# Optimization experiments

Hardware: AMD Instinct MI355X
Metric: run time of the kernel (lower is better)

Reference implementation:

```python
import jax, jax.numpy as jnp
import numpy as np

N_INT4, N_INT8, K, GROUP = 6144, 2048, 8192, 128
N_TOTAL = N_INT4 + N_INT8
M = 16


def setup_inputs() -> dict:
    key = jax.random.key(0)
    ks = jax.random.split(key, 8)
    x = jax.random.normal(ks[0], (M, K), jnp.float32)
    # uint4 weights: values 0..15 (stored int32)
    w_int4 = jax.random.randint(ks[1], (N_INT4, K), 0, 16, jnp.int32)
    # group-wise scales [N_int4, K//group_size]
    s_int4 = jax.random.uniform(ks[2], (N_INT4, K // GROUP), jnp.float32, minval=0.005, maxval=0.02)
    # int8 weights stored in offset-128 form (w_int8 + 128 -> 0..255), as pack_for_marlin builds
    w_uint8 = jax.random.randint(ks[3], (N_INT8, K), 0, 256, jnp.int32)
    # per-channel int8 scales
    s_int8 = jax.random.uniform(ks[4], (N_INT8,), jnp.float32, minval=0.005, maxval=0.02)
    awq_scales = jax.random.uniform(ks[5], (K,), jnp.float32, minval=0.5, maxval=2.0)
    bias = jax.random.normal(ks[6], (N_TOTAL,), jnp.float32) * 0.01
    inv_perm = jax.random.permutation(ks[7], N_TOTAL).astype(jnp.int32)
    return dict(x=x, w_int4=w_int4, s_int4=s_int4, w_uint8=w_uint8, s_int8=s_int8,
                awq_scales=awq_scales, bias=bias, inv_perm=inv_perm, group_size=GROUP)


def reference(x, w_int4, s_int4, w_uint8, s_int8, awq_scales, bias, inv_perm, group_size):
    dt = x.dtype
    k = x.shape[-1]
    # AWQ input scaling (unfused path: x / awq_scales)
    x2 = x.reshape(-1, k) / awq_scales[None, :]
    sum_x = jnp.sum(x2, axis=1, keepdims=True)  # [M, 1]

    # Marlin uint4b8 dequant: (q - 8) * scale, group-wise scales for int4 rows
    s4_k = jnp.repeat(s_int4, group_size, axis=1)            # [N4, K]
    W4 = (w_int4.astype(dt) - 8.0) * s4_k                    # [N4, K]

    # int8 rows split into high/low nibbles with scales 16*s and s
    high = (w_uint8 >> 4) & 15
    low = w_uint8 & 15
    Wh = (high.astype(dt) - 8.0) * (16.0 * s_int8)[:, None]  # [N8, K]
    Wl = (low.astype(dt) - 8.0) * s_int8[:, None]            # [N8, K]

    Wc = jnp.concatenate([W4, Wh, Wl], axis=0)               # [N4+2*N8, K]
    y = x2 @ Wc.T                                            # marlin_gemm equivalent

    n4 = W4.shape[0]
    n8 = s_int8.shape[0]
    y4 = y[:, :n4]
    # int8 reconstruction: y_high + y_low + 8*s_int8*sum_x  == s_int8 * (x @ w_int8^T)
    y8 = y[:, n4:n4 + n8] + y[:, n4 + n8:] + (8.0 * s_int8)[None, :] * sum_x
    y_out = jnp.concatenate([y4, y8], axis=-1)[:, inv_perm] + bias[None, :]
    return y_out.reshape(*x.shape[:-1], n4 + n8)
```

## Files before the change

### kernel.cpp

```cpp
#include <hip/hip_runtime.h>
#include <hip/hip_bf16.h>

constexpr int K    = 8192;
constexpr int N4   = 6144;
constexpr int N8   = 2048;
constexpr int NT   = N4 + N8;
constexpr int NG   = K / 128;
constexpr int SPLITS = 16;
constexpr int CPS    = 16;

typedef short  short8  __attribute__((ext_vector_type(8)));
typedef float  floatx4 __attribute__((ext_vector_type(4)));

__device__ inline short f2bf(float f) {
    __hip_bfloat16 h = __float2bfloat16(f);
    return __builtin_bit_cast(short, h);
}

__global__ void prep_kernel(const float* __restrict__ x,
                            const float* __restrict__ awq,
                            const int*   __restrict__ inv_perm,
                            const float* __restrict__ bias,
                            short* __restrict__ x2bf,
                            int*   __restrict__ fwd,
                            float* __restrict__ out) {
    const int tid  = blockIdx.x * blockDim.x + threadIdx.x;
    const int c    = tid >> 9;
    const int rem  = tid & 511;
    const int lane = rem >> 3;
    const int j    = rem & 7;
    const int m    = lane & 15;
    const int k    = c * 32 + (lane >> 4) * 8 + j;
    x2bf[tid] = f2bf(x[m * K + k] / awq[k]);
    out[tid]  = bias[tid & (NT - 1)];
    if (tid < NT) fwd[inv_perm[tid]] = tid;
}

__global__ __launch_bounds__(256)
void qgemv_kernel(const short* __restrict__ xf,
                  const int*   __restrict__ w4,
                  const float* __restrict__ s4,
                  const int*   __restrict__ w8,
                  const float* __restrict__ s8,
                  const int*   __restrict__ fwd,
                  float* __restrict__ out) {
    const int t    = threadIdx.x;
    const int lane = t & 63;
    const int wid  = blockIdx.x * 4 + (t >> 6);
    const int tile = wid >> 4;
    const int spl  = wid & (SPLITS - 1);
    const int nb   = tile * 16;
    const int i    = lane & 15;
    const int q    = lane >> 4;
    const int row  = nb + i;

    const bool is4 = (nb < N4);
    const int* wr  = is4 ? (w4 + (size_t)row * K + q * 8)
                         : (w8 + (size_t)(row - N4) * K + q * 8);
    const int c0   = spl * CPS;

    floatx4 acc = {0.f, 0.f, 0.f, 0.f};

    #pragma unroll 1
    for (int gi = 0; gi < 4; ++gi) {
        const int g   = (c0 >> 2) + gi;
        const float s  = is4 ? s4[row * NG + g] : 1.f;
        const float sb = is4 ? -8.f * s : -128.f;

        #pragma unroll
        for (int ci = 0; ci < 4; ++ci) {
            const int c = c0 + gi * 4 + ci;
            const int4 wa = *(const int4*)(wr + (size_t)c * 32);
            const int4 wb = *(const int4*)(wr + (size_t)c * 32 + 4);

            short8 bfrag;
            bfrag[0] = f2bf((float)wa.x * s + sb);
            bfrag[1] = f2bf((float)wa.y * s + sb);
            bfrag[2] = f2bf((float)wa.z * s + sb);
            bfrag[3] = f2bf((float)wa.w * s + sb);
            bfrag[4] = f2bf((float)wb.x * s + sb);
            bfrag[5] = f2bf((float)wb.y * s + sb);
            bfrag[6] = f2bf((float)wb.z * s + sb);
            bfrag[7] = f2bf((float)wb.w * s + sb);

            const short8 afrag = *(const short8*)(xf + (size_t)c * 512 + lane * 8);

            acc = __builtin_amdgcn_mfma_f32_16x16x32_bf16(afrag, bfrag, acc, 0, 0, 0);
        }
    }

    const float sc = is4 ? 1.f : s8[row - N4];
    const int   d  = fwd[row];
    #pragma unroll
    for (int r = 0; r < 4; ++r) {
        const int m = q * 4 + r;
        unsafeAtomicAdd(&out[(size_t)m * NT + d], acc[r] * sc);
    }
}

extern "C" void kernel_launch(void* const* d_in, const int* in_sizes, int n_in,
                              void* d_out, int out_size, void* d_ws, size_t ws_size,
                              hipStream_t stream) {
    const float* x        = (const float*)d_in[0];
    const int*   w_int4   = (const int*)  d_in[1];
    const float* s_int4   = (const float*)d_in[2];
    const int*   w_uint8  = (const int*)  d_in[3];
    const float* s_int8   = (const float*)d_in[4];
    const float* awq      = (const float*)d_in[5];
    const float* bias     = (const float*)d_in[6];
    const int*   inv_perm = (const int*)  d_in[7];

    short* x2bf = (short*)d_ws;
    int*   fwd  = (int*)((char*)d_ws + (size_t)16 * K * sizeof(short));

    prep_kernel<<<(16 * K) / 256, 256, 0, stream>>>(x, awq, inv_perm, bias,
                                                    x2bf, fwd, (float*)d_out);
    qgemv_kernel<<<2048, 256, 0, stream>>>(x2bf, w_int4, s_int4,
                                           w_uint8, s_int8, fwd,
                                           (float*)d_out);
}
```

Measured before the change: 370.5 us.

## Reduce split-K within a block via LDS and double-buffer loads

Each block now owns one 16-row tile and splits K across its four waves. Partial sums are reduced through shared memory instead of global atomics, and the bias add moves from the prep kernel into the final store. The main loop double-buffers weight and activation loads per scale group to overlap memory with dequant and MFMA work. The grid shrinks from 2048 to 512 blocks, so each wave streams a longer K range. That cuts parallelism and may leave fewer loads in flight for this bandwidth-bound read of int32 weights.

```diff
diff --git a/kernel.cpp b/kernel.cpp
--- a/kernel.cpp
+++ b/kernel.cpp
@@ -6,8 +6,6 @@
 constexpr int N8   = 2048;
 constexpr int NT   = N4 + N8;
 constexpr int NG   = K / 128;
-constexpr int SPLITS = 16;
-constexpr int CPS    = 16;
 
 typedef short  short8  __attribute__((ext_vector_type(8)));
 typedef float  floatx4 __attribute__((ext_vector_type(4)));
@@ -20,10 +18,8 @@
 __global__ void prep_kernel(const float* __restrict__ x,
                             const float* __restrict__ awq,
                             const int*   __restrict__ inv_perm,
-                            const float* __restrict__ bias,
                             short* __restrict__ x2bf,
-                            int*   __restrict__ fwd,
-                            float* __restrict__ out) {
+                            int*   __restrict__ fwd) {
     const int tid  = blockIdx.x * blockDim.x + threadIdx.x;
     const int c    = tid >> 9;
     const int rem  = tid & 511;
@@ -32,7 +28,6 @@
     const int m    = lane & 15;
     const int k    = c * 32 + (lane >> 4) * 8 + j;
     x2bf[tid] = f2bf(x[m * K + k] / awq[k]);
-    out[tid]  = bias[tid & (NT - 1)];
     if (tid < NT) fwd[inv_perm[tid]] = tid;
 }
 
@@ -43,58 +38,87 @@
                   const int*   __restrict__ w8,
                   const float* __restrict__ s8,
                   const int*   __restrict__ fwd,
+                  const float* __restrict__ bias,
                   float* __restrict__ out) {
+    __shared__ float lds[4 * 256];
+
     const int t    = threadIdx.x;
     const int lane = t & 63;
-    const int wid  = blockIdx.x * 4 + (t >> 6);
-    const int tile = wid >> 4;
-    const int spl  = wid & (SPLITS - 1);
-    const int nb   = tile * 16;
+    const int w    = t >> 6;
+    const int nb   = blockIdx.x * 16;
     const int i    = lane & 15;
     const int q    = lane >> 4;
     const int row  = nb + i;
 
     const bool is4 = (nb < N4);
-    const int* wr  = is4 ? (w4 + (size_t)row * K + q * 8)
-                         : (w8 + (size_t)(row - N4) * K + q * 8);
-    const int c0   = spl * CPS;
+    const int*   wp = (is4 ? (w4 + (size_t)row * K)
+                           : (w8 + (size_t)(row - N4) * K))
+                      + (size_t)w * 2048 + q * 8;
+    const short* xw = xf + (size_t)w * 64 * 512 + lane * 8;
+    const float* sp = is4 ? (s4 + (size_t)row * NG + w * 16) : nullptr;
 
     floatx4 acc = {0.f, 0.f, 0.f, 0.f};
 
+    int4   wbA[8], wbB[8];
+    short8 abA[4], abB[4];
+    float  sA = 0.f, sB = 0.f;
+
+    auto loadg = [&](int g, int4* wb, short8* ab, float& s) {
+        #pragma unroll
+        for (int c = 0; c < 4; ++c) {
+            const size_t co = (size_t)(g * 4 + c);
+            wb[2 * c]     = *(const int4*)(wp + co * 32);
+            wb[2 * c + 1] = *(const int4*)(wp + co * 32 + 4);
+            ab[c]         = *(const short8*)(xw + co * 512);
+        }
+        if (is4) s = sp[g];
+    };
+
+    auto compg = [&](const int4* wb, const short8* ab, float s) {
+        const float sc = is4 ? s : 1.f;
+        const float sb = is4 ? -8.f * s : -128.f;
+        #pragma unroll
+        for (int c = 0; c < 4; ++c) {
+            const int4 wa = wb[2 * c];
+            const int4 wz = wb[2 * c + 1];
+            short8 bf;
+            bf[0] = f2bf((float)wa.x * sc + sb);
+            bf[1] = f2bf((float)wa.y * sc + sb);
+            bf[2] = f2bf((float)wa.z * sc + sb);
+            bf[3] = f2bf((float)wa.w * sc + sb);
+            bf[4] = f2bf((float)wz.x * sc + sb);
+            bf[5] = f2bf((float)wz.y * sc + sb);
+            bf[6] = f2bf((float)wz.z * sc + sb);
+            bf[7] = f2bf((float)wz.w * sc + sb);
+            acc = __builtin_amdgcn_mfma_f32_16x16x32_bf16(ab[c], bf, acc, 0, 0, 0);
+        }
+    };
+
+    loadg(0, wbA, abA, sA);
     #pragma unroll 1
-    for (int gi = 0; gi < 4; ++gi) {
-        const int g   = (c0 >> 2) + gi;
-        const float s  = is4 ? s4[row * NG + g] : 1.f;
-        const float sb = is4 ? -8.f * s : -128.f;
-
-        #pragma unroll
-        for (int ci = 0; ci < 4; ++ci) {
-            const int c = c0 + gi * 4 + ci;
-            const int4 wa = *(const int4*)(wr + (size_t)c * 32);
-            const int4 wb = *(const int4*)(wr + (size_t)c * 32 + 4);
-
-            short8 bfrag;
-            bfrag[0] = f2bf((float)wa.x * s + sb);
-            bfrag[1] = f2bf((float)wa.y * s + sb);
-            bfrag[2] = f2bf((float)wa.z * s + sb);
-            bfrag[3] = f2bf((float)wa.w * s + sb);
-            bfrag[4] = f2bf((float)wb.x * s + sb);
-            bfrag[5] = f2bf((float)wb.y * s + sb);
-            bfrag[6] = f2bf((float)wb.z * s + sb);
-            bfrag[7] = f2bf((float)wb.w * s + sb);
-
-            const short8 afrag = *(const short8*)(xf + (size_t)c * 512 + lane * 8);
-
-            acc = __builtin_amdgcn_mfma_f32_16x16x32_bf16(afrag, bfrag, acc, 0, 0, 0);
-        }
+    for (int g = 0; g < 16; g += 2) {
+        const int g1 = (g + 1 < 16) ? g + 1 : 15;
+        loadg(g1, wbB, abB, sB);
+        compg(wbA, abA, sA);
+        const int g2 = (g + 2 < 16) ? g + 2 : 15;
+        loadg(g2, wbA, abA, sA);
+        compg(wbB, abB, sB);
     }
 
-    const float sc = is4 ? 1.f : s8[row - N4];
-    const int   d  = fwd[row];
     #pragma unroll
-    for (int r = 0; r < 4; ++r) {
-        const int m = q * 4 + r;
-        unsafeAtomicAdd(&out[(size_t)m * NT + d], acc[r] * sc);
+    for (int r = 0; r < 4; ++r)
+        lds[w * 256 + (q * 4 + r) * 16 + i] = acc[r];
+    __syncthreads();
+
+    {
+        const int m  = t >> 4;
+        const int i2 = t & 15;
+        const float v = lds[0 * 256 + t] + lds[1 * 256 + t]
+                      + lds[2 * 256 + t] + lds[3 * 256 + t];
+        const int n  = nb + i2;
+        const float sc = is4 ? 1.f : s8[n - N4];
+        const int d  = fwd[n];
+        out[(size_t)m * NT + d] = v * sc + bias[d];
     }
 }
 
@@ -113,9 +137,8 @@
     short* x2bf = (short*)d_ws;
     int*   fwd  = (int*)((char*)d_ws + (size_t)16 * K * sizeof(short));
 
-    prep_kernel<<<(16 * K) / 256, 256, 0, stream>>>(x, awq, inv_perm, bias,
-                                                    x2bf, fwd, (float*)d_out);
-    qgemv_kernel<<<2048, 256, 0, stream>>>(x2bf, w_int4, s_int4,
-                                           w_uint8, s_int8, fwd,
-                                           (float*)d_out);
+    prep_kernel<<<(16 * K) / 256, 256, 0, stream>>>(x, awq, inv_perm, x2bf, fwd);
+    qgemv_kernel<<<NT / 16, 256, 0, stream>>>(x2bf, w_int4, s_int4,
+                                              w_uint8, s_int8, fwd, bias,
+                                              (float*)d_out);
 }
```

After: 337.3 us. -9.0%, faster.

## Stage weight tiles into LDS via async global_load_lds double buffering

Applied to the files above, without the earlier changes.

Restructures the GEMV so each block handles a 16-row tile over half of K. It streams weight rows into a double-buffered LDS tile with global_load_lds DMA while the four waves compute on the previous buffer. Group scales are now applied after each MFMA on integer-offset bf16 values rather than during dequant. Partial sums are reduced in LDS before the atomics, which cuts the atomic count. In exchange it adds two __syncthreads per iteration, roughly 33KB of LDS per block, and half as many blocks, which may limit memory parallelism.

```diff
diff --git a/kernel.cpp b/kernel.cpp
--- a/kernel.cpp
+++ b/kernel.cpp
@@ -6,15 +6,20 @@
 constexpr int N8   = 2048;
 constexpr int NT   = N4 + N8;
 constexpr int NG   = K / 128;
-constexpr int SPLITS = 16;
-constexpr int CPS    = 16;
+constexpr int WSTR = 258;
 
 typedef short  short8  __attribute__((ext_vector_type(8)));
 typedef float  floatx4 __attribute__((ext_vector_type(4)));
+typedef __attribute__((address_space(1))) void gas_t;
+typedef __attribute__((address_space(3))) void las_t;
 
 __device__ inline short f2bf(float f) {
     __hip_bfloat16 h = __float2bfloat16(f);
     return __builtin_bit_cast(short, h);
+}
+
+__device__ __forceinline__ void dma16(const void* g, void* l) {
+    __builtin_amdgcn_global_load_lds((gas_t*)g, (las_t*)l, 16, 0, 0);
 }
 
 __global__ void prep_kernel(const float* __restrict__ x,
@@ -36,6 +41,20 @@
     if (tid < NT) fwd[inv_perm[tid]] = tid;
 }
 
+__device__ __forceinline__ floatx4 chunk_mfma(int4 wa, int4 wb, short8 xv,
+                                              float off, floatx4 cin) {
+    short8 bf;
+    bf[0] = f2bf((float)wa.x + off);
+    bf[1] = f2bf((float)wa.y + off);
+    bf[2] = f2bf((float)wa.z + off);
+    bf[3] = f2bf((float)wa.w + off);
+    bf[4] = f2bf((float)wb.x + off);
+    bf[5] = f2bf((float)wb.y + off);
+    bf[6] = f2bf((float)wb.z + off);
+    bf[7] = f2bf((float)wb.w + off);
+    return __builtin_amdgcn_mfma_f32_16x16x32_bf16(xv, bf, cin, 0, 0, 0);
+}
+
 __global__ __launch_bounds__(256)
 void qgemv_kernel(const short* __restrict__ xf,
                   const int*   __restrict__ w4,
@@ -44,57 +63,77 @@
                   const float* __restrict__ s8,
                   const int*   __restrict__ fwd,
                   float* __restrict__ out) {
+    __shared__ int   wbuf[2][16 * WSTR];
+    __shared__ float red[4][256];
+
     const int t    = threadIdx.x;
     const int lane = t & 63;
-    const int wid  = blockIdx.x * 4 + (t >> 6);
-    const int tile = wid >> 4;
-    const int spl  = wid & (SPLITS - 1);
+    const int w    = t >> 6;
+    const int tile = blockIdx.x >> 1;
+    const int spl  = blockIdx.x & 1;
     const int nb   = tile * 16;
     const int i    = lane & 15;
     const int q    = lane >> 4;
     const int row  = nb + i;
 
-    const bool is4 = (nb < N4);
-    const int* wr  = is4 ? (w4 + (size_t)row * K + q * 8)
-                         : (w8 + (size_t)(row - N4) * K + q * 8);
-    const int c0   = spl * CPS;
+    const bool  is4 = (nb < N4);
+    const float off = is4 ? -8.f : -128.f;
+    const float s8row = is4 ? 0.f : s8[row - N4];
+    const int   kb  = spl * 4096;
+
+    const int* wbase = is4 ? (w4 + (size_t)nb * K) : (w8 + (size_t)(nb - N4) * K);
 
     floatx4 acc = {0.f, 0.f, 0.f, 0.f};
 
-    #pragma unroll 1
-    for (int gi = 0; gi < 4; ++gi) {
-        const int g   = (c0 >> 2) + gi;
-        const float s  = is4 ? s4[row * NG + g] : 1.f;
-        const float sb = is4 ? -8.f * s : -128.f;
-
-        #pragma unroll
-        for (int ci = 0; ci < 4; ++ci) {
-            const int c = c0 + gi * 4 + ci;
-            const int4 wa = *(const int4*)(wr + (size_t)c * 32);
-            const int4 wb = *(const int4*)(wr + (size_t)c * 32 + 4);
-
-            short8 bfrag;
-            bfrag[0] = f2bf((float)wa.x * s + sb);
-            bfrag[1] = f2bf((float)wa.y * s + sb);
-            bfrag[2] = f2bf((float)wa.z * s + sb);
-            bfrag[3] = f2bf((float)wa.w * s + sb);
-            bfrag[4] = f2bf((float)wb.x * s + sb);
-            bfrag[5] = f2bf((float)wb.y * s + sb);
-            bfrag[6] = f2bf((float)wb.z * s + sb);
-            bfrag[7] = f2bf((float)wb.w * s + sb);
-
-            const short8 afrag = *(const short8*)(xf + (size_t)c * 512 + lane * 8);
-
-            acc = __builtin_amdgcn_mfma_f32_16x16x32_bf16(afrag, bfrag, acc, 0, 0, 0);
-        }
+    #pragma unroll
+    for (int a = 0; a < 4; ++a) {
+        const int r = w + 4 * a;
+        dma16(wbase + (size_t)r * K + kb + lane * 4, &wbuf[0][r * WSTR]);
     }
 
-    const float sc = is4 ? 1.f : s8[row - N4];
-    const int   d  = fwd[row];
+    #pragma unroll 1
+    for (int it = 0; it < 16; ++it) {
+        const int nxt = (it + 1 < 16) ? it + 1 : 15;
+        #pragma unroll
+        for (int a = 0; a < 4; ++a) {
+            const int r = w + 4 * a;
+            dma16(wbase + (size_t)r * K + kb + nxt * 256 + lane * 4,
+                  &wbuf[(it + 1) & 1][r * WSTR]);
+        }
+
+        const int   g  = spl * 32 + it * 2 + (w >> 1);
+        const float sg = is4 ? s4[(size_t)row * NG + g] : s8row;
+
+        __syncthreads();
+
+        const int* wb = &wbuf[it & 1][0];
+        floatx4 gacc = {0.f, 0.f, 0.f, 0.f};
+        #pragma unroll
+        for (int cc = 0; cc < 2; ++cc) {
+            const int c   = 2 * w + cc;
+            const int4 wv0 = *(const int4*)(wb + i * WSTR + c * 32 + q * 8);
+            const int4 wv1 = *(const int4*)(wb + i * WSTR + c * 32 + q * 8 + 4);
+            const short8 xv = *(const short8*)(xf + (size_t)(spl * 128 + it * 8 + c) * 512
+                                               + lane * 8);
+            gacc = chunk_mfma(wv0, wv1, xv, off, gacc);
+        }
+        acc[0] += sg * gacc[0]; acc[1] += sg * gacc[1];
+        acc[2] += sg * gacc[2]; acc[3] += sg * gacc[3];
+
+        __syncthreads();
+    }
+
     #pragma unroll
-    for (int r = 0; r < 4; ++r) {
-        const int m = q * 4 + r;
-        unsafeAtomicAdd(&out[(size_t)m * NT + d], acc[r] * sc);
+    for (int r = 0; r < 4; ++r)
+        red[w][(q * 4 + r) * 16 + i] = acc[r];
+    __syncthreads();
+
+    if (t < 256) {
+        const float v = red[0][t] + red[1][t] + red[2][t] + red[3][t];
+        const int m  = t >> 4;
+        const int i2 = t & 15;
+        const int d  = fwd[nb + i2];
+        unsafeAtomicAdd(&out[(size_t)m * NT + d], v);
     }
 }
 
@@ -115,7 +154,7 @@
 
     prep_kernel<<<(16 * K) / 256, 256, 0, stream>>>(x, awq, inv_perm, bias,
                                                     x2bf, fwd, (float*)d_out);
-    qgemv_kernel<<<2048, 256, 0, stream>>>(x2bf, w_int4, s_int4,
+    qgemv_kernel<<<1024, 256, 0, stream>>>(x2bf, w_int4, s_int4,
                                            w_uint8, s_int8, fwd,
                                            (float*)d_out);
 }
```

Result: faster. 338.0 us (-8.8%).
